# Kernel tuning notes

Hardware: AMD Instinct MI355X
Metric: run time of the kernel (lower is better)

Reference implementation:

```python
import jax, jax.numpy as jnp
import numpy as np

ETA = 0.15
LAM = 0.05
K = 6


def setup_inputs() -> dict:
    key = jax.random.key(0)
    ks = jax.random.split(key, 9)
    Bsz, L, d, hidden = 32, 8192, 64, 256
    scale = lambda fan_in: 1.0 / np.sqrt(fan_in)
    return {
        "A": jax.random.normal(ks[0], (Bsz, L, d), jnp.float32),
        "B": jax.random.normal(ks[1], (Bsz, L, d), jnp.float32),
        "q": jax.random.normal(ks[2], (Bsz, L, d), jnp.float32),
        "W1": jax.random.normal(ks[3], (2 * d, hidden), jnp.float32) * scale(2 * d),
        "b1": jax.random.normal(ks[4], (hidden,), jnp.float32) * 0.01,
        "W2": jax.random.normal(ks[5], (hidden, d), jnp.float32) * scale(hidden),
        "b2": jax.random.normal(ks[6], (d,), jnp.float32) * 0.01,
        "Wq": jax.random.normal(ks[7], (d, d), jnp.float32) * scale(d),
        "bq": jax.random.normal(ks[8], (d,), jnp.float32) * 0.01,
    }


def _smooth1d(x):
    return x - LAM * (2.0 * x - jnp.roll(x, 1, axis=1) - jnp.roll(x, -1, axis=1))


def reference(A, B, q, W1, b1, W2, b2, Wq, bq):
    # mu_net: Linear -> ReLU -> Linear -> Softplus on concat([A,B])
    h = jnp.concatenate([A, B], axis=-1)  # [B, L, 2d]
    mu = jax.nn.softplus(jax.nn.relu(h @ W1 + b1) @ W2 + b2)  # [B, L, d]
    gate = jnp.tanh(q @ Wq + bq)
    mu = mu * (1.0 + 0.5 * gate)

    hA, hB = A, B
    for _ in range(K):
        step = ETA * (mu * (hA - hB))
        hA = _smooth1d(hA - step)
        hB = _smooth1d(hB + step)

    energy = 0.5 * jnp.sum(mu * jnp.square(hA - hB), axis=(1, 2))  # [B]
    return hA, hB, energy
```

## Files before the change

kernel.cpp:

```cpp
#include <hip/hip_runtime.h>
#include <hip/hip_bf16.h>
#include <hip/hip_fp16.h>

#define ETA 0.15f
#define LAM 0.05f

typedef unsigned int uint32;
typedef __attribute__((ext_vector_type(8))) short short8;
typedef __attribute__((ext_vector_type(4))) float floatx4;
typedef __attribute__((ext_vector_type(4))) _Float16 half4;

static const int BSZ = 32, LL = 8192, DD = 64;
static const int RTOT = BSZ * LL;

static const size_t MU_BYTES = (size_t)RTOT * DD * 2;
static const size_t W1T_OFF  = MU_BYTES;
static const size_t W2T_OFF  = W1T_OFF + 256 * 128 * 2;
static const size_t WQT_OFF  = W2T_OFF + 64 * 256 * 2;

__device__ __forceinline__ unsigned short f2bf(float f) {
    uint32 u = __builtin_bit_cast(uint32, f);
    uint32 r = (u + 0x7FFFu + ((u >> 16) & 1u)) >> 16;
    return (unsigned short)r;
}
__device__ __forceinline__ float fast_softplus(float x) {
    return fmaxf(x, 0.f) + __logf(1.f + __expf(-fabsf(x)));
}
__device__ __forceinline__ float fast_tanh(float x) {
    float t = __expf(-2.f * fabsf(x));
    float r = (1.f - t) / (1.f + t);
    return copysignf(r, x);
}

__global__ void prep_kernel(const float* __restrict__ W1, const float* __restrict__ W2,
                            const float* __restrict__ Wq,
                            unsigned short* __restrict__ w1t, unsigned short* __restrict__ w2t,
                            unsigned short* __restrict__ wqt, float* __restrict__ energy) {
    int tid = blockIdx.x * blockDim.x + threadIdx.x;
    int nth = gridDim.x * blockDim.x;
    for (int i = tid; i < 256 * 128; i += nth) { int n = i >> 7, k = i & 127; w1t[i] = f2bf(W1[k * 256 + n]); }
    for (int i = tid; i < 64 * 256; i += nth) { int n = i >> 8, k = i & 255; w2t[i] = f2bf(W2[k * 64 + n]); }
    for (int i = tid; i < 64 * 64;  i += nth) { int n = i >> 6, k = i & 63;  wqt[i] = f2bf(Wq[k * 64 + n]); }
    if (tid < 32) energy[tid] = 0.f;
}

__global__ __launch_bounds__(256) void mlp_kernel(
    const float* __restrict__ A, const float* __restrict__ B, const float* __restrict__ Q,
    const float* __restrict__ b1, const float* __restrict__ b2, const float* __restrict__ bq,
    const unsigned short* __restrict__ w1t, const unsigned short* __restrict__ w2t,
    const unsigned short* __restrict__ wqt, _Float16* __restrict__ mu_out) {
    __shared__ char lds[34816];
    unsigned short* Xs = (unsigned short*)(lds);
    unsigned short* Qs = (unsigned short*)(lds + 17408);
    unsigned short* Zs = (unsigned short*)(lds);

    const int tid = threadIdx.x;
    const int lane = tid & 63;
    const int w = tid >> 6;
    const int q4 = lane >> 4;
    const int l16 = lane & 15;
    const int rowbase = blockIdx.x * 64;

    uint32* Xu = (uint32*)Xs;
    for (int i = tid; i < 64 * 64; i += 256) {
        int r = i >> 6, j2 = i & 63;
        const float* src = (j2 < 32) ? (A + (size_t)(rowbase + r) * 64 + 2 * j2)
                                     : (B + (size_t)(rowbase + r) * 64 + 2 * (j2 - 32));
        float2 v = *(const float2*)src;
        Xu[r * 68 + j2] = (uint32)f2bf(v.x) | ((uint32)f2bf(v.y) << 16);
    }
    uint32* Qu = (uint32*)Qs;
    for (int i = tid; i < 64 * 32; i += 256) {
        int r = i >> 5, j2 = i & 31;
        float2 v = *(const float2*)(Q + (size_t)(rowbase + r) * 64 + 2 * j2);
        Qu[r * 36 + j2] = (uint32)f2bf(v.x) | ((uint32)f2bf(v.y) << 16);
    }
    __syncthreads();

    floatx4 acc3[4];
#pragma unroll
    for (int m = 0; m < 4; m++) acc3[m] = (floatx4){0.f, 0.f, 0.f, 0.f};
    {
        short8 wqf[2];
#pragma unroll
        for (int kt = 0; kt < 2; kt++)
            wqf[kt] = *(const short8*)&wqt[(w * 16 + l16) * 64 + kt * 32 + q4 * 8];
#pragma unroll
        for (int m = 0; m < 4; m++)
#pragma unroll
            for (int kt = 0; kt < 2; kt++) {
                short8 aq = *(const short8*)&Qs[(m * 16 + l16) * 72 + kt * 32 + q4 * 8];
                acc3[m] = __builtin_amdgcn_mfma_f32_16x16x32_bf16(aq, wqf[kt], acc3[m], 0, 0, 0);
            }
    }
    short8 ax[4][4];
#pragma unroll
    for (int m = 0; m < 4; m++)
#pragma unroll
        for (int kt = 0; kt < 4; kt++)
            ax[m][kt] = *(const short8*)&Xs[(m * 16 + l16) * 136 + kt * 32 + q4 * 8];
    __syncthreads();

#pragma unroll
    for (int nt = 0; nt < 4; nt++) {
        const int ng = w * 4 + nt;
        short8 wf[4];
#pragma unroll
        for (int kt = 0; kt < 4; kt++)
            wf[kt] = *(const short8*)&w1t[(ng * 16 + l16) * 128 + kt * 32 + q4 * 8];
        floatx4 acc[4];
#pragma unroll
        for (int m = 0; m < 4; m++) acc[m] = (floatx4){0.f, 0.f, 0.f, 0.f};
#pragma unroll
        for (int kt = 0; kt < 4; kt++)
#pragma unroll
            for (int m = 0; m < 4; m++)
                acc[m] = __builtin_amdgcn_mfma_f32_16x16x32_bf16(ax[m][kt], wf[kt], acc[m], 0, 0, 0);
        const int col = ng * 16 + l16;
        const float b1v = b1[col];
#pragma unroll
        for (int m = 0; m < 4; m++)
#pragma unroll
            for (int r = 0; r < 4; r++) {
                float z = acc[m][r] + b1v;
                z = z > 0.f ? z : 0.f;
                Zs[(m * 16 + q4 * 4 + r) * 272 + col] = f2bf(z);
            }
    }
    short8 w2f[8];
#pragma unroll
    for (int kt = 0; kt < 8; kt++)
        w2f[kt] = *(const short8*)&w2t[(w * 16 + l16) * 256 + kt * 32 + q4 * 8];
    __syncthreads();

    floatx4 acc2[4];
#pragma unroll
    for (int m = 0; m < 4; m++) acc2[m] = (floatx4){0.f, 0.f, 0.f, 0.f};
#pragma unroll
    for (int m = 0; m < 4; m++)
#pragma unroll
        for (int kt = 0; kt < 8; kt++) {
            short8 az = *(const short8*)&Zs[(m * 16 + l16) * 272 + kt * 32 + q4 * 8];
            acc2[m] = __builtin_amdgcn_mfma_f32_16x16x32_bf16(az, w2f[kt], acc2[m], 0, 0, 0);
        }
    const int col = w * 16 + l16;
    const float b2v = b2[col], bqv = bq[col];
#pragma unroll
    for (int m = 0; m < 4; m++)
#pragma unroll
        for (int r = 0; r < 4; r++) {
            int row = m * 16 + q4 * 4 + r;
            float sp = fast_softplus(acc2[m][r] + b2v);
            float g = fast_tanh(acc3[m][r] + bqv);
            float mu = sp * (1.f + 0.5f * g);
            mu_out[(size_t)(rowbase + row) * 64 + col] = (_Float16)mu;
        }
}

__global__ __launch_bounds__(256) void iter_kernel(
    const float* __restrict__ A, const float* __restrict__ B, const _Float16* __restrict__ mu_ws,
    float* __restrict__ outA, float* __restrict__ outB, float* __restrict__ energy) {
    __shared__ float ex[2][4][16][64];
    __shared__ float esm[4];
    const int tid = threadIdx.x;
    const int c4 = tid & 15;
    const int g = tid >> 4;
    const int b = blockIdx.y;
    const int s = blockIdx.x * 64;
    const size_t bbase = (size_t)b * 8192;
    const int r0 = g * 5;

    floatx4 a[5], bv[5], me[5];
#pragma unroll
    for (int i = 0; i < 5; i++) {
        int gl = (s + r0 + i + 8192 - 8) & 8191;
        size_t base = (bbase + gl) * 64 + c4 * 4;
        a[i] = *(const floatx4*)(A + base);
        bv[i] = *(const floatx4*)(B + base);
        half4 m4 = *(const half4*)(mu_ws + base);
        me[i] = __builtin_convertvector(m4, floatx4) * ETA;
    }
    for (int it = 0; it < 6; it++) {
#pragma unroll
        for (int i = 0; i < 5; i++) {
            floatx4 st = me[i] * (a[i] - bv[i]);
            a[i] = a[i] - st;
            bv[i] = bv[i] + st;
        }
        const int p = it & 1;
        *(floatx4*)&ex[p][0][g][c4 * 4] = a[0];
        *(floatx4*)&ex[p][1][g][c4 * 4] = a[4];
        *(floatx4*)&ex[p][2][g][c4 * 4] = bv[0];
        *(floatx4*)&ex[p][3][g][c4 * 4] = bv[4];
        __syncthreads();
        floatx4 aUp = (g > 0)  ? *(const floatx4*)&ex[p][1][g - 1][c4 * 4] : a[0];
        floatx4 aDn = (g < 15) ? *(const floatx4*)&ex[p][0][g + 1][c4 * 4] : a[4];
        floatx4 bUp = (g > 0)  ? *(const floatx4*)&ex[p][3][g - 1][c4 * 4] : bv[0];
        floatx4 bDn = (g < 15) ? *(const floatx4*)&ex[p][2][g + 1][c4 * 4] : bv[4];
        floatx4 prev = aUp, cur = a[0];
#pragma unroll
        for (int i = 0; i < 5; i++) {
            floatx4 nxt = (i < 4) ? a[i + 1] : aDn;
            a[i] = cur - LAM * (2.f * cur - prev - nxt);
            prev = cur; cur = nxt;
        }
        prev = bUp; cur = bv[0];
#pragma unroll
        for (int i = 0; i < 5; i++) {
            floatx4 nxt = (i < 4) ? bv[i + 1] : bDn;
            bv[i] = cur - LAM * (2.f * cur - prev - nxt);
            prev = cur; cur = nxt;
        }
    }
    float e = 0.f;
#pragma unroll
    for (int i = 0; i < 5; i++) {
        int wr = r0 + i;
        if (wr >= 8 && wr < 72) {
            floatx4 d = a[i] - bv[i];
            floatx4 q = me[i] * d * d;
            e += q.x + q.y + q.z + q.w;
            size_t gidx = (bbase + s + (wr - 8)) * 64 + c4 * 4;
            *(floatx4*)(outA + gidx) = a[i];
            *(floatx4*)(outB + gidx) = bv[i];
        }
    }
    e *= 0.5f / ETA;
#pragma unroll
    for (int off = 32; off > 0; off >>= 1) e += __shfl_down(e, off, 64);
    if ((tid & 63) == 0) esm[tid >> 6] = e;
    __syncthreads();
    if (tid == 0) atomicAdd(energy + b, esm[0] + esm[1] + esm[2] + esm[3]);
}

extern "C" void kernel_launch(void* const* d_in, const int* in_sizes, int n_in,
                              void* d_out, int out_size, void* d_ws, size_t ws_size,
                              hipStream_t stream) {
    const float* A  = (const float*)d_in[0];
    const float* B  = (const float*)d_in[1];
    const float* Q  = (const float*)d_in[2];
    const float* W1 = (const float*)d_in[3];
    const float* b1 = (const float*)d_in[4];
    const float* W2 = (const float*)d_in[5];
    const float* b2 = (const float*)d_in[6];
    const float* Wq = (const float*)d_in[7];
    const float* bq = (const float*)d_in[8];

    float* outA = (float*)d_out;
    float* outB = outA + (size_t)RTOT * 64;
    float* energy = outB + (size_t)RTOT * 64;

    char* ws = (char*)d_ws;
    _Float16* mu_ws = (_Float16*)ws;
    unsigned short* w1t = (unsigned short*)(ws + W1T_OFF);
    unsigned short* w2t = (unsigned short*)(ws + W2T_OFF);
    unsigned short* wqt = (unsigned short*)(ws + WQT_OFF);

    hipLaunchKernelGGL(prep_kernel, dim3(64), dim3(256), 0, stream,
                       W1, W2, Wq, w1t, w2t, wqt, energy);
    hipLaunchKernelGGL(mlp_kernel, dim3(RTOT / 64), dim3(256), 0, stream,
                       A, B, Q, b1, b2, bq, w1t, w2t, wqt, mu_ws);
    hipLaunchKernelGGL(iter_kernel, dim3(LL / 64, BSZ), dim3(256), 0, stream,
                       A, B, mu_ws, outA, outB, energy);
}
```

Measured before the change: 411.9 us.

## Reformulate iteration in sum/difference basis and tune MLP staging, swizzle, priorities

The iteration kernel now tracks s=A+B and d=A-B, so each step only scales d by a precomputed factor (1-2·ETA·mu) and smooths both. This removes per-step subtraction and multiply work, and A and B are rebuilt only at the end. The MLP kernel gains several changes: float4 loads with packed bf16 conversion via v_cvt_pk_bf16_f32, and an XOR-swizzled unpadded Z layout in LDS to avoid bank conflicts. It also hoists weight and bias loads and raises wave priority around MFMA blocks with s_setprio. The new algebra changes rounding slightly and moves energy scaling into the factor.

```diff
diff --git a/kernel.cpp b/kernel.cpp
--- a/kernel.cpp
+++ b/kernel.cpp
@@ -8,6 +8,7 @@
 typedef unsigned int uint32;
 typedef __attribute__((ext_vector_type(8))) short short8;
 typedef __attribute__((ext_vector_type(4))) float floatx4;
+typedef __attribute__((ext_vector_type(2))) uint32 uint32x2;
 typedef __attribute__((ext_vector_type(4))) _Float16 half4;
 
 static const int BSZ = 32, LL = 8192, DD = 64;
@@ -22,6 +23,11 @@
     uint32 u = __builtin_bit_cast(uint32, f);
     uint32 r = (u + 0x7FFFu + ((u >> 16) & 1u)) >> 16;
     return (unsigned short)r;
+}
+__device__ __forceinline__ uint32 cvtpk(float lo, float hi) {
+    uint32 r;
+    asm("v_cvt_pk_bf16_f32 %0, %1, %2" : "=v"(r) : "v"(lo), "v"(hi));
+    return r;
 }
 __device__ __forceinline__ float fast_softplus(float x) {
     return fmaxf(x, 0.f) + __logf(1.f + __expf(-fabsf(x)));
@@ -49,7 +55,7 @@
     const float* __restrict__ b1, const float* __restrict__ b2, const float* __restrict__ bq,
     const unsigned short* __restrict__ w1t, const unsigned short* __restrict__ w2t,
     const unsigned short* __restrict__ wqt, _Float16* __restrict__ mu_out) {
-    __shared__ char lds[34816];
+    __shared__ char lds[32768];
     unsigned short* Xs = (unsigned short*)(lds);
     unsigned short* Qs = (unsigned short*)(lds + 17408);
     unsigned short* Zs = (unsigned short*)(lds);
@@ -61,38 +67,46 @@
     const int l16 = lane & 15;
     const int rowbase = blockIdx.x * 64;
 
+    short8 wqf[2];
+#pragma unroll
+    for (int kt = 0; kt < 2; kt++)
+        wqf[kt] = *(const short8*)&wqt[(w * 16 + l16) * 64 + kt * 32 + q4 * 8];
+    float b1v4[4];
+#pragma unroll
+    for (int nt = 0; nt < 4; nt++) b1v4[nt] = b1[(w * 4 + nt) * 16 + l16];
+    const int ocol = w * 16 + l16;
+    const float b2v = b2[ocol], bqv = bq[ocol];
+
     uint32* Xu = (uint32*)Xs;
-    for (int i = tid; i < 64 * 64; i += 256) {
-        int r = i >> 6, j2 = i & 63;
-        const float* src = (j2 < 32) ? (A + (size_t)(rowbase + r) * 64 + 2 * j2)
-                                     : (B + (size_t)(rowbase + r) * 64 + 2 * (j2 - 32));
-        float2 v = *(const float2*)src;
-        Xu[r * 68 + j2] = (uint32)f2bf(v.x) | ((uint32)f2bf(v.y) << 16);
+    for (int i = tid; i < 64 * 32; i += 256) {
+        int r = i >> 5, c = i & 31;
+        const float* src = (c < 16) ? (A + (size_t)(rowbase + r) * 64 + c * 4)
+                                    : (B + (size_t)(rowbase + r) * 64 + (c - 16) * 4);
+        floatx4 v = *(const floatx4*)src;
+        uint32x2 u; u.x = cvtpk(v.x, v.y); u.y = cvtpk(v.z, v.w);
+        *(uint32x2*)&Xu[r * 68 + c * 2] = u;
     }
     uint32* Qu = (uint32*)Qs;
-    for (int i = tid; i < 64 * 32; i += 256) {
-        int r = i >> 5, j2 = i & 31;
-        float2 v = *(const float2*)(Q + (size_t)(rowbase + r) * 64 + 2 * j2);
-        Qu[r * 36 + j2] = (uint32)f2bf(v.x) | ((uint32)f2bf(v.y) << 16);
+    for (int i = tid; i < 64 * 16; i += 256) {
+        int r = i >> 4, c = i & 15;
+        floatx4 v = *(const floatx4*)(Q + (size_t)(rowbase + r) * 64 + c * 4);
+        uint32x2 u; u.x = cvtpk(v.x, v.y); u.y = cvtpk(v.z, v.w);
+        *(uint32x2*)&Qu[r * 36 + c * 2] = u;
     }
     __syncthreads();
 
     floatx4 acc3[4];
 #pragma unroll
     for (int m = 0; m < 4; m++) acc3[m] = (floatx4){0.f, 0.f, 0.f, 0.f};
-    {
-        short8 wqf[2];
-#pragma unroll
-        for (int kt = 0; kt < 2; kt++)
-            wqf[kt] = *(const short8*)&wqt[(w * 16 + l16) * 64 + kt * 32 + q4 * 8];
-#pragma unroll
-        for (int m = 0; m < 4; m++)
-#pragma unroll
-            for (int kt = 0; kt < 2; kt++) {
-                short8 aq = *(const short8*)&Qs[(m * 16 + l16) * 72 + kt * 32 + q4 * 8];
-                acc3[m] = __builtin_amdgcn_mfma_f32_16x16x32_bf16(aq, wqf[kt], acc3[m], 0, 0, 0);
-            }
-    }
+    __builtin_amdgcn_s_setprio(1);
+#pragma unroll
+    for (int m = 0; m < 4; m++)
+#pragma unroll
+        for (int kt = 0; kt < 2; kt++) {
+            short8 aq = *(const short8*)&Qs[(m * 16 + l16) * 72 + kt * 32 + q4 * 8];
+            acc3[m] = __builtin_amdgcn_mfma_f32_16x16x32_bf16(aq, wqf[kt], acc3[m], 0, 0, 0);
+        }
+    __builtin_amdgcn_s_setprio(0);
     short8 ax[4][4];
 #pragma unroll
     for (int m = 0; m < 4; m++)
@@ -111,21 +125,31 @@
         floatx4 acc[4];
 #pragma unroll
         for (int m = 0; m < 4; m++) acc[m] = (floatx4){0.f, 0.f, 0.f, 0.f};
+        __builtin_amdgcn_s_setprio(1);
 #pragma unroll
         for (int kt = 0; kt < 4; kt++)
 #pragma unroll
             for (int m = 0; m < 4; m++)
                 acc[m] = __builtin_amdgcn_mfma_f32_16x16x32_bf16(ax[m][kt], wf[kt], acc[m], 0, 0, 0);
+        __builtin_amdgcn_s_setprio(0);
         const int col = ng * 16 + l16;
-        const float b1v = b1[col];
-#pragma unroll
-        for (int m = 0; m < 4; m++)
-#pragma unroll
-            for (int r = 0; r < 4; r++) {
-                float z = acc[m][r] + b1v;
-                z = z > 0.f ? z : 0.f;
-                Zs[(m * 16 + q4 * 4 + r) * 272 + col] = f2bf(z);
-            }
+        const int c8 = col >> 3, c7 = col & 7;
+        const float b1v = b1v4[nt];
+#pragma unroll
+        for (int m = 0; m < 4; m++) {
+            float z0 = fmaxf(acc[m][0] + b1v, 0.f);
+            float z1 = fmaxf(acc[m][1] + b1v, 0.f);
+            float z2 = fmaxf(acc[m][2] + b1v, 0.f);
+            float z3 = fmaxf(acc[m][3] + b1v, 0.f);
+            uint32 u01 = cvtpk(z0, z1), u23 = cvtpk(z2, z3);
+            const int row0 = m * 16 + q4 * 4;
+            const int a0 = row0 * 256 + ((c8 ^ (q4 * 2)) << 3) + c7;
+            const int a2 = (row0 + 2) * 256 + ((c8 ^ (q4 * 2 + 1)) << 3) + c7;
+            Zs[a0]       = (unsigned short)u01;
+            Zs[a0 + 256] = (unsigned short)(u01 >> 16);
+            Zs[a2]       = (unsigned short)u23;
+            Zs[a2 + 256] = (unsigned short)(u23 >> 16);
+        }
     }
     short8 w2f[8];
 #pragma unroll
@@ -136,15 +160,16 @@
     floatx4 acc2[4];
 #pragma unroll
     for (int m = 0; m < 4; m++) acc2[m] = (floatx4){0.f, 0.f, 0.f, 0.f};
+    const int sxr = (l16 >> 1) & 7;
+    __builtin_amdgcn_s_setprio(1);
 #pragma unroll
     for (int m = 0; m < 4; m++)
 #pragma unroll
         for (int kt = 0; kt < 8; kt++) {
-            short8 az = *(const short8*)&Zs[(m * 16 + l16) * 272 + kt * 32 + q4 * 8];
+            short8 az = *(const short8*)&Zs[(m * 16 + l16) * 256 + (((kt * 4 + q4) ^ sxr) << 3)];
             acc2[m] = __builtin_amdgcn_mfma_f32_16x16x32_bf16(az, w2f[kt], acc2[m], 0, 0, 0);
         }
-    const int col = w * 16 + l16;
-    const float b2v = b2[col], bqv = bq[col];
+    __builtin_amdgcn_s_setprio(0);
 #pragma unroll
     for (int m = 0; m < 4; m++)
 #pragma unroll
@@ -153,7 +178,7 @@
             float sp = fast_softplus(acc2[m][r] + b2v);
             float g = fast_tanh(acc3[m][r] + bqv);
             float mu = sp * (1.f + 0.5f * g);
-            mu_out[(size_t)(rowbase + row) * 64 + col] = (_Float16)mu;
+            mu_out[(size_t)(rowbase + row) * 64 + ocol] = (_Float16)mu;
         }
 }
 
@@ -166,49 +191,48 @@
     const int c4 = tid & 15;
     const int g = tid >> 4;
     const int b = blockIdx.y;
-    const int s = blockIdx.x * 64;
+    const int s0 = blockIdx.x * 64;
     const size_t bbase = (size_t)b * 8192;
     const int r0 = g * 5;
 
-    floatx4 a[5], bv[5], me[5];
+    floatx4 sv[5], dv[5], fv[5];
 #pragma unroll
     for (int i = 0; i < 5; i++) {
-        int gl = (s + r0 + i + 8192 - 8) & 8191;
+        int gl = (s0 + r0 + i + 8192 - 8) & 8191;
         size_t base = (bbase + gl) * 64 + c4 * 4;
-        a[i] = *(const floatx4*)(A + base);
-        bv[i] = *(const floatx4*)(B + base);
+        floatx4 av = *(const floatx4*)(A + base);
+        floatx4 bv = *(const floatx4*)(B + base);
         half4 m4 = *(const half4*)(mu_ws + base);
-        me[i] = __builtin_convertvector(m4, floatx4) * ETA;
+        floatx4 mu = __builtin_convertvector(m4, floatx4);
+        sv[i] = av + bv;
+        dv[i] = av - bv;
+        fv[i] = 1.f - (2.f * ETA) * mu;
     }
     for (int it = 0; it < 6; it++) {
 #pragma unroll
+        for (int i = 0; i < 5; i++) dv[i] *= fv[i];
+        const int p = it & 1;
+        *(floatx4*)&ex[p][0][g][c4 * 4] = sv[0];
+        *(floatx4*)&ex[p][1][g][c4 * 4] = sv[4];
+        *(floatx4*)&ex[p][2][g][c4 * 4] = dv[0];
+        *(floatx4*)&ex[p][3][g][c4 * 4] = dv[4];
+        __syncthreads();
+        floatx4 sUp = (g > 0)  ? *(const floatx4*)&ex[p][1][g - 1][c4 * 4] : sv[0];
+        floatx4 sDn = (g < 15) ? *(const floatx4*)&ex[p][0][g + 1][c4 * 4] : sv[4];
+        floatx4 dUp = (g > 0)  ? *(const floatx4*)&ex[p][3][g - 1][c4 * 4] : dv[0];
+        floatx4 dDn = (g < 15) ? *(const floatx4*)&ex[p][2][g + 1][c4 * 4] : dv[4];
+        floatx4 prev = sUp, cur = sv[0];
+#pragma unroll
         for (int i = 0; i < 5; i++) {
-            floatx4 st = me[i] * (a[i] - bv[i]);
-            a[i] = a[i] - st;
-            bv[i] = bv[i] + st;
-        }
-        const int p = it & 1;
-        *(floatx4*)&ex[p][0][g][c4 * 4] = a[0];
-        *(floatx4*)&ex[p][1][g][c4 * 4] = a[4];
-        *(floatx4*)&ex[p][2][g][c4 * 4] = bv[0];
-        *(floatx4*)&ex[p][3][g][c4 * 4] = bv[4];
-        __syncthreads();
-        floatx4 aUp = (g > 0)  ? *(const floatx4*)&ex[p][1][g - 1][c4 * 4] : a[0];
-        floatx4 aDn = (g < 15) ? *(const floatx4*)&ex[p][0][g + 1][c4 * 4] : a[4];
-        floatx4 bUp = (g > 0)  ? *(const floatx4*)&ex[p][3][g - 1][c4 * 4] : bv[0];
-        floatx4 bDn = (g < 15) ? *(const floatx4*)&ex[p][2][g + 1][c4 * 4] : bv[4];
-        floatx4 prev = aUp, cur = a[0];
+            floatx4 nxt = (i < 4) ? sv[i + 1] : sDn;
+            sv[i] = cur - LAM * (2.f * cur - prev - nxt);
+            prev = cur; cur = nxt;
+        }
+        prev = dUp; cur = dv[0];
 #pragma unroll
         for (int i = 0; i < 5; i++) {
-            floatx4 nxt = (i < 4) ? a[i + 1] : aDn;
-            a[i] = cur - LAM * (2.f * cur - prev - nxt);
-            prev = cur; cur = nxt;
-        }
-        prev = bUp; cur = bv[0];
-#pragma unroll
-        for (int i = 0; i < 5; i++) {
-            floatx4 nxt = (i < 4) ? bv[i + 1] : bDn;
-            bv[i] = cur - LAM * (2.f * cur - prev - nxt);
+            floatx4 nxt = (i < 4) ? dv[i + 1] : dDn;
+            dv[i] = cur - LAM * (2.f * cur - prev - nxt);
             prev = cur; cur = nxt;
         }
     }
@@ -217,15 +241,15 @@
     for (int i = 0; i < 5; i++) {
         int wr = r0 + i;
         if (wr >= 8 && wr < 72) {
-            floatx4 d = a[i] - bv[i];
-            floatx4 q = me[i] * d * d;
+            floatx4 d = dv[i];
+            floatx4 q = (1.f - fv[i]) * d * d;
             e += q.x + q.y + q.z + q.w;
-            size_t gidx = (bbase + s + (wr - 8)) * 64 + c4 * 4;
-            *(floatx4*)(outA + gidx) = a[i];
-            *(floatx4*)(outB + gidx) = bv[i];
-        }
-    }
-    e *= 0.5f / ETA;
+            size_t gidx = (bbase + s0 + (wr - 8)) * 64 + c4 * 4;
+            *(floatx4*)(outA + gidx) = (sv[i] + d) * 0.5f;
+            *(floatx4*)(outB + gidx) = (sv[i] - d) * 0.5f;
+        }
+    }
+    e *= 0.25f / ETA;
 #pragma unroll
     for (int off = 32; off > 0; off >>= 1) e += __shfl_down(e, off, 64);
     if ((tid & 63) == 0) esm[tid >> 6] = e;
```

Result: faster. 396.1 us (-3.8%).
